# Optimization experiments

Hardware: AMD Instinct MI355X
Metric: run time of the kernel (lower is better)

The kernel has to match this reference:

```python
import jax, jax.numpy as jnp
import numpy as np

H = 512  # hidden_size
HGT, WID = 256, 256


def setup_inputs() -> dict:
    key = jax.random.key(0)
    k1, k2, k3, k4, k5, k6, k7 = jax.random.split(key, 7)
    s_att = 1.0 / np.sqrt(2 * H)
    s_ctx = 1.0 / np.sqrt(2 * H)
    return {
        "inp": jax.random.normal(k1, (1, 1, H), dtype=jnp.float32),
        "hid": jax.random.normal(k2, (1, 1, H), dtype=jnp.float32),
        "V": jax.random.normal(k3, (HGT, WID, H), dtype=jnp.float32),
        "att_w": jax.random.uniform(k4, (1, 2 * H), jnp.float32, -s_att, s_att),
        "att_b": jax.random.uniform(k5, (1,), jnp.float32, -s_att, s_att),
        "ctx_w": jax.random.uniform(k6, (H, 2 * H), jnp.float32, -s_ctx, s_ctx),
        "ctx_b": jax.random.uniform(k7, (H,), jnp.float32, -s_ctx, s_ctx),
    }


def reference(inp, hid, V, att_w, att_b, ctx_w, ctx_b):
    # attention Linear over concat(hid, V[i,j]) -> split weight into two halves
    w_hid = att_w[0, :H]   # applied to hid[0,0] (same for all positions)
    w_v = att_w[0, H:]     # applied to V[i,j]
    hid_term = jnp.dot(hid[0, 0], w_hid) + att_b[0]           # scalar
    alpha = jnp.einsum('ijk,k->ij', V, w_v) + hid_term        # [h, w]
    alpha = jax.nn.softmax(alpha.reshape(-1)).reshape(alpha.shape)
    attn = jnp.einsum('ij,ijk->k', alpha, V)                  # [H]
    cat = jnp.concatenate([inp[0, 0], attn])                  # [2H]
    ctx = jax.nn.relu(cat @ ctx_w.T + ctx_b)                  # [H]
    return ctx[None, None, :]                                 # [1, 1, H]
```

## Files before the change

### kernel.cpp

```cpp
#include <hip/hip_runtime.h>


#define HDIM 512
#define NPOS 65536

__device__ __forceinline__ float wave_sum(float v) {
#pragma unroll
    for (int m = 32; m >= 1; m >>= 1) v += __shfl_xor(v, m, 64);
    return v;
}

__global__ __launch_bounds__(256, 4)
void k1_partial(const float* __restrict__ V, const float* __restrict__ att_w,
                float* __restrict__ ws1, int B) {
    const int tid  = threadIdx.x;
    const int lane = tid & 63;
    const int wid  = tid >> 6;
    const int b    = blockIdx.x;
    const int gw   = b * 4 + wid;
    const int W    = B * 4;
    const int niter = NPOS / W;

    const float* wvp = att_w + HDIM + lane * 8;
    const float4 wv0 = *reinterpret_cast<const float4*>(wvp);
    const float4 wv1 = *reinterpret_cast<const float4*>(wvp + 4);

    float acc[8] = {0.f,0.f,0.f,0.f,0.f,0.f,0.f,0.f};
    float lsum = 0.f;

#pragma unroll 2
    for (int it = 0; it < niter; ++it) {
        const int p = gw + it * W;
        const float* vp = V + (size_t)p * HDIM + lane * 8;
        const float4 a0 = *reinterpret_cast<const float4*>(vp);
        const float4 a1 = *reinterpret_cast<const float4*>(vp + 4);
        float d = a0.x*wv0.x + a0.y*wv0.y + a0.z*wv0.z + a0.w*wv0.w;
        d      += a1.x*wv1.x + a1.y*wv1.y + a1.z*wv1.z + a1.w*wv1.w;
        d = wave_sum(d);
        const float e = __expf(d);
        lsum += e;
        acc[0] += e*a0.x; acc[1] += e*a0.y; acc[2] += e*a0.z; acc[3] += e*a0.w;
        acc[4] += e*a1.x; acc[5] += e*a1.y; acc[6] += e*a1.z; acc[7] += e*a1.w;
    }

    __shared__ float lds[4][HDIM];
    __shared__ float ldsl[4];
#pragma unroll
    for (int j = 0; j < 8; ++j) lds[wid][lane*8 + j] = acc[j];
    if (lane == 0) ldsl[wid] = lsum;
    __syncthreads();

    const float s0 = lds[0][tid]       + lds[1][tid]       + lds[2][tid]       + lds[3][tid];
    const float s1 = lds[0][tid + 256] + lds[1][tid + 256] + lds[2][tid + 256] + lds[3][tid + 256];
    float* dst = ws1 + (size_t)b * 513;
    dst[tid]       = s0;
    dst[tid + 256] = s1;
    if (tid == 0) dst[512] = ldsl[0] + ldsl[1] + ldsl[2] + ldsl[3];
}

__global__ __launch_bounds__(256)
void k2_combine(const float* __restrict__ ws1, float* __restrict__ ws2, int B) {
    const int lane = threadIdx.x & 63;
    const int wid  = threadIdx.x >> 6;
    const int k = blockIdx.x * 4 + wid;
    if (k > 512) return;
    float s = 0.f;
    for (int bb = lane; bb < B; bb += 64) s += ws1[(size_t)bb * 513 + k];
    s = wave_sum(s);
    if (lane == 0) ws2[k] = s;
}

__global__ __launch_bounds__(256)
void k3_fc(const float* __restrict__ inp, const float* __restrict__ ctx_w,
           const float* __restrict__ ctx_b, const float* __restrict__ ws2,
           float* __restrict__ out) {
    const int lane = threadIdx.x & 63;
    const int wid  = threadIdx.x >> 6;
    const int r = blockIdx.x * 4 + wid;
    const float invL = 1.0f / ws2[512];
    const int cbase = lane * 16;

    float4 c0, c1, c2, c3;
    if (lane < 32) {
        const float* p = inp + cbase;
        c0 = *reinterpret_cast<const float4*>(p);
        c1 = *reinterpret_cast<const float4*>(p + 4);
        c2 = *reinterpret_cast<const float4*>(p + 8);
        c3 = *reinterpret_cast<const float4*>(p + 12);
    } else {
        const float* p = ws2 + (cbase - HDIM);
        c0 = *reinterpret_cast<const float4*>(p);
        c1 = *reinterpret_cast<const float4*>(p + 4);
        c2 = *reinterpret_cast<const float4*>(p + 8);
        c3 = *reinterpret_cast<const float4*>(p + 12);
        c0.x *= invL; c0.y *= invL; c0.z *= invL; c0.w *= invL;
        c1.x *= invL; c1.y *= invL; c1.z *= invL; c1.w *= invL;
        c2.x *= invL; c2.y *= invL; c2.z *= invL; c2.w *= invL;
        c3.x *= invL; c3.y *= invL; c3.z *= invL; c3.w *= invL;
    }

    const float* w = ctx_w + (size_t)r * 1024 + cbase;
    const float4 w0 = *reinterpret_cast<const float4*>(w);
    const float4 w1 = *reinterpret_cast<const float4*>(w + 4);
    const float4 w2 = *reinterpret_cast<const float4*>(w + 8);
    const float4 w3 = *reinterpret_cast<const float4*>(w + 12);

    float d = c0.x*w0.x + c0.y*w0.y + c0.z*w0.z + c0.w*w0.w;
    d      += c1.x*w1.x + c1.y*w1.y + c1.z*w1.z + c1.w*w1.w;
    d      += c2.x*w2.x + c2.y*w2.y + c2.z*w2.z + c2.w*w2.w;
    d      += c3.x*w3.x + c3.y*w3.y + c3.z*w3.z + c3.w*w3.w;
    d = wave_sum(d);
    if (lane == 0) out[r] = fmaxf(d + ctx_b[r], 0.0f);
}

extern "C" void kernel_launch(void* const* d_in, const int* in_sizes, int n_in,
                              void* d_out, int out_size, void* d_ws, size_t ws_size,
                              hipStream_t stream) {
    const float* inp   = (const float*)d_in[0];
    const float* V     = (const float*)d_in[2];
    const float* att_w = (const float*)d_in[3];
    const float* ctx_w = (const float*)d_in[5];
    const float* ctx_b = (const float*)d_in[6];
    float* out = (float*)d_out;
    float* ws  = (float*)d_ws;

    int B = 1024;
    while (B > 64 && ((size_t)B * 513 + 513) * sizeof(float) > ws_size) B >>= 1;

    float* ws1 = ws;
    float* ws2 = ws + (size_t)B * 513;

    k1_partial<<<dim3(B),   dim3(256), 0, stream>>>(V, att_w, ws1, B);
    k2_combine<<<dim3(129), dim3(256), 0, stream>>>(ws1, ws2, B);
    k3_fc     <<<dim3(128), dim3(256), 0, stream>>>(inp, ctx_w, ctx_b, ws2, out);
}
```

Baseline: 209.6 us.

## Widen partial-softmax blocks to 8 waves and split combine into two-stage reduction

The streaming kernel now uses 512-thread blocks (8 waves) with a fixed 1024-block grid, which doubles the number of resident waves reading V and halves the iterations per wave. The per-block LDS reduction uses vectorised float4 stores. The cross-block combine is replaced by a two-stage reduction, 64 blocks of 16 rows each followed by a single block, with coalesced column reads instead of strided per-wave gathers. In exchange it adds an extra kernel launch, and the workspace size check is removed, so it assumes ws is large enough.

```diff
diff --git a/kernel.cpp b/kernel.cpp
--- a/kernel.cpp
+++ b/kernel.cpp
@@ -3,6 +3,9 @@
 
 #define HDIM 512
 #define NPOS 65536
+#define B1   1024
+#define W1   (B1*8)
+#define NITER (NPOS / W1)
 
 __device__ __forceinline__ float wave_sum(float v) {
 #pragma unroll
@@ -10,16 +13,13 @@
     return v;
 }
 
-__global__ __launch_bounds__(256, 4)
+__global__ __launch_bounds__(512, 8)
 void k1_partial(const float* __restrict__ V, const float* __restrict__ att_w,
-                float* __restrict__ ws1, int B) {
+                float* __restrict__ ws1) {
     const int tid  = threadIdx.x;
     const int lane = tid & 63;
     const int wid  = tid >> 6;
-    const int b    = blockIdx.x;
-    const int gw   = b * 4 + wid;
-    const int W    = B * 4;
-    const int niter = NPOS / W;
+    const int gw   = blockIdx.x * 8 + wid;
 
     const float* wvp = att_w + HDIM + lane * 8;
     const float4 wv0 = *reinterpret_cast<const float4*>(wvp);
@@ -29,8 +29,8 @@
     float lsum = 0.f;
 
 #pragma unroll 2
-    for (int it = 0; it < niter; ++it) {
-        const int p = gw + it * W;
+    for (int it = 0; it < NITER; ++it) {
+        const int p = gw + it * W1;
         const float* vp = V + (size_t)p * HDIM + lane * 8;
         const float4 a0 = *reinterpret_cast<const float4*>(vp);
         const float4 a1 = *reinterpret_cast<const float4*>(vp + 4);
@@ -43,31 +43,65 @@
         acc[4] += e*a1.x; acc[5] += e*a1.y; acc[6] += e*a1.z; acc[7] += e*a1.w;
     }
 
-    __shared__ float lds[4][HDIM];
-    __shared__ float ldsl[4];
-#pragma unroll
-    for (int j = 0; j < 8; ++j) lds[wid][lane*8 + j] = acc[j];
+    __shared__ float lds[8][HDIM];
+    __shared__ float ldsl[8];
+    float4* lv = reinterpret_cast<float4*>(&lds[wid][lane * 8]);
+    lv[0] = make_float4(acc[0], acc[1], acc[2], acc[3]);
+    lv[1] = make_float4(acc[4], acc[5], acc[6], acc[7]);
     if (lane == 0) ldsl[wid] = lsum;
     __syncthreads();
 
-    const float s0 = lds[0][tid]       + lds[1][tid]       + lds[2][tid]       + lds[3][tid];
-    const float s1 = lds[0][tid + 256] + lds[1][tid + 256] + lds[2][tid + 256] + lds[3][tid + 256];
-    float* dst = ws1 + (size_t)b * 513;
-    dst[tid]       = s0;
-    dst[tid + 256] = s1;
-    if (tid == 0) dst[512] = ldsl[0] + ldsl[1] + ldsl[2] + ldsl[3];
+    float s = 0.f;
+#pragma unroll
+    for (int w = 0; w < 8; ++w) s += lds[w][tid];
+    float* dst = ws1 + (size_t)blockIdx.x * 513;
+    dst[tid] = s;
+    if (tid == 0) {
+        float t = 0.f;
+#pragma unroll
+        for (int w = 0; w < 8; ++w) t += ldsl[w];
+        dst[512] = t;
+    }
 }
 
 __global__ __launch_bounds__(256)
-void k2_combine(const float* __restrict__ ws1, float* __restrict__ ws2, int B) {
-    const int lane = threadIdx.x & 63;
-    const int wid  = threadIdx.x >> 6;
-    const int k = blockIdx.x * 4 + wid;
-    if (k > 512) return;
-    float s = 0.f;
-    for (int bb = lane; bb < B; bb += 64) s += ws1[(size_t)bb * 513 + k];
-    s = wave_sum(s);
-    if (lane == 0) ws2[k] = s;
+void k2a(const float* __restrict__ ws1, float* __restrict__ ws1b) {
+    const int g = blockIdx.x;
+    const int t = threadIdx.x;
+    const float* base = ws1 + (size_t)g * 16 * 513;
+#pragma unroll
+    for (int half = 0; half < 2; ++half) {
+        const int c = t + half * 256;
+        float s = 0.f;
+#pragma unroll
+        for (int r = 0; r < 16; ++r) s += base[r * 513 + c];
+        ws1b[g * 513 + c] = s;
+    }
+    if (t == 0) {
+        float s = 0.f;
+#pragma unroll
+        for (int r = 0; r < 16; ++r) s += base[r * 513 + 512];
+        ws1b[g * 513 + 512] = s;
+    }
+}
+
+__global__ __launch_bounds__(256)
+void k2b(const float* __restrict__ ws1b, float* __restrict__ ws2) {
+    const int t = threadIdx.x;
+#pragma unroll
+    for (int half = 0; half < 2; ++half) {
+        const int c = t + half * 256;
+        float s = 0.f;
+#pragma unroll
+        for (int g = 0; g < 64; ++g) s += ws1b[g * 513 + c];
+        ws2[c] = s;
+    }
+    if (t == 0) {
+        float s = 0.f;
+#pragma unroll
+        for (int g = 0; g < 64; ++g) s += ws1b[g * 513 + 512];
+        ws2[512] = s;
+    }
 }
 
 __global__ __launch_bounds__(256)
@@ -124,13 +158,12 @@
     float* out = (float*)d_out;
     float* ws  = (float*)d_ws;
 
-    int B = 1024;
-    while (B > 64 && ((size_t)B * 513 + 513) * sizeof(float) > ws_size) B >>= 1;
+    float* ws1  = ws;
+    float* ws1b = ws1 + (size_t)B1 * 513;
+    float* ws2  = ws1b + (size_t)64 * 513;
 
-    float* ws1 = ws;
-    float* ws2 = ws + (size_t)B * 513;
-
-    k1_partial<<<dim3(B),   dim3(256), 0, stream>>>(V, att_w, ws1, B);
-    k2_combine<<<dim3(129), dim3(256), 0, stream>>>(ws1, ws2, B);
-    k3_fc     <<<dim3(128), dim3(256), 0, stream>>>(inp, ctx_w, ctx_b, ws2, out);
+    k1_partial<<<dim3(B1), dim3(512), 0, stream>>>(V, att_w, ws1);
+    k2a       <<<dim3(64), dim3(256), 0, stream>>>(ws1, ws1b);
+    k2b       <<<dim3(1),  dim3(256), 0, stream>>>(ws1b, ws2);
+    k3_fc     <<<dim3(128),dim3(256), 0, stream>>>(inp, ctx_w, ctx_b, ws2, out);
 }
```

Measured after the change: 212.6 us. No clear change (+1.4%).
